# Kernel optimization log

Hardware: AMD Instinct MI355X
Metric: run time of the kernel (lower is better)

Reference implementation:

```python
import jax, jax.numpy as jnp
import numpy as np

B, S, D, R = 8, 2048, 2048, 4  # batch, seq, dim, n_roles


def setup_inputs() -> dict:
    key = jax.random.key(0)
    k1, k2, k3 = jax.random.split(key, 3)
    hidden = jax.random.normal(k1, (B, S, D), dtype=jnp.float32)
    roles = jax.random.randint(k2, (B,), 0, R)
    role_onehot = jax.nn.one_hot(roles, R, dtype=jnp.float32)  # [B, R]
    # per-role Linear params (nn.Linear(dim, dim)), Kaiming-ish init scale
    W = jax.random.normal(k3, (R, D, D), dtype=jnp.float32) / np.sqrt(D)
    b = jnp.zeros((R, D), dtype=jnp.float32)
    scales = jnp.ones((R,), dtype=jnp.float32)  # role_scales
    return {"hidden": hidden, "role_onehot": role_onehot, "W": W, "b": b, "scales": scales}


def reference(hidden, role_onehot, W, b, scales):
    # Training path: compute every role's Linear+Tanh*scale, then mask-sum by one-hot.
    # transformed: [R, B, S, D]
    t = jnp.tanh(jnp.einsum('bsd,rde->rbse', hidden, W) + b[:, None, None, :])
    t = t * scales[:, None, None, None]
    # weights = role_onehot^T broadcast over (S, D); sum over roles
    return jnp.einsum('rbse,br->bse', t, role_onehot)
```

## Files before the change

kernel.cpp:

```cpp
#include <hip/hip_runtime.h>
#include <stdint.h>


#define BDIM 8
#define SDIM 2048
#define DDIM 2048
#define RDIM 4

typedef __attribute__((ext_vector_type(8))) short bf16x8;
typedef __attribute__((ext_vector_type(4))) float f32x4;
typedef unsigned int uint32;

__device__ __forceinline__ unsigned short f2bf(float f) {
    uint32 u = __float_as_uint(f);
    u += 0x7fffu + ((u >> 16) & 1u);
    return (unsigned short)(u >> 16);
}
__device__ __forceinline__ uint32 pack2(float lo, float hi) {
    return (uint32)f2bf(lo) | ((uint32)f2bf(hi) << 16);
}
__device__ __forceinline__ float fast_tanh(float x) {
    float ax = __builtin_fabsf(x);
    float e = __expf(-2.0f * ax);
    float t = (1.0f - e) * __builtin_amdgcn_rcpf(1.0f + e);
    return __builtin_copysignf(t, x);
}


__global__ __launch_bounds__(256) void cvt_h_kernel(const float* __restrict__ h,
                                                    unsigned short* __restrict__ o, int n8) {
    int i = blockIdx.x * blockDim.x + threadIdx.x;
    int stride = gridDim.x * blockDim.x;
    for (; i < n8; i += stride) {
        float4 v0 = reinterpret_cast<const float4*>(h)[2 * i];
        float4 v1 = reinterpret_cast<const float4*>(h)[2 * i + 1];
        uint4 p;
        p.x = pack2(v0.x, v0.y);
        p.y = pack2(v0.z, v0.w);
        p.z = pack2(v1.x, v1.y);
        p.w = pack2(v1.z, v1.w);
        reinterpret_cast<uint4*>(o)[i] = p;
    }
}

__global__ __launch_bounds__(256) void cvt_wt_kernel(const float* __restrict__ w,
                                                     unsigned short* __restrict__ o) {
    __shared__ unsigned short tile[64][65];
    int r = blockIdx.z;
    int e0 = blockIdx.x * 64, d0 = blockIdx.y * 64;
    const float* wr = w + (size_t)r * DDIM * DDIM;
    unsigned short* orr = o + (size_t)r * DDIM * DDIM;
    int tx = threadIdx.x & 63, ty = threadIdx.x >> 6;
    #pragma unroll
    for (int i = ty; i < 64; i += 4)
        tile[i][tx] = f2bf(wr[(size_t)(d0 + i) * DDIM + e0 + tx]);
    __syncthreads();
    #pragma unroll
    for (int i = ty; i < 64; i += 4)
        orr[(size_t)(e0 + i) * DDIM + d0 + tx] = tile[tx][i];
}


__global__ __launch_bounds__(512, 2) void role_gemm8(
    const unsigned short* __restrict__ Hb,
    const unsigned short* __restrict__ Wt,
    const float* __restrict__ onehot,
    const float* __restrict__ bias,
    const float* __restrict__ scales,
    float* __restrict__ out)
{
    constexpr int NT = DDIM / 64;
    extern __shared__ char lds[];

    const int tid = threadIdx.x;
    const int l = tid & 63;
    const int wv = tid >> 6;
    const int wm = wv >> 2;
    const int wn = wv & 3;
    const int fr = l & 15;
    const int fq = l >> 4;
    const int l7 = l & 7;
    const int colx0 = ((fq ^ l7) << 4);
    const int colx1 = (((4 + fq) ^ l7) << 4);

    int bid = blockIdx.x;
    int swz = (bid & 7) * 64 + (bid >> 3);
    int batch = swz >> 6;
    int tt = swz & 63;
    int row0 = (tt >> 3) * 256;
    int n0 = (tt & 7) * 256;

    int role = 0;
    #pragma unroll
    for (int r = 1; r < RDIM; ++r) role = (onehot[batch * RDIM + r] > 0.5f) ? r : role;

    const unsigned short* A = Hb + (size_t)batch * SDIM * DDIM;
    const unsigned short* Bw = Wt + (size_t)role * DDIM * DDIM;

    f32x4 acc[8][4];
    #pragma unroll
    for (int m = 0; m < 8; ++m)
        #pragma unroll
        for (int n = 0; n < 4; ++n)
            #pragma unroll
            for (int j = 0; j < 4; ++j) acc[m][n][j] = 0.0f;

    bf16x8 aR[4][2];
    bf16x8 bQ0[2][2];
    bf16x8 bQ1[2][2];

    auto stage_half = [&](int d, int kind, int h, int T) {
        const unsigned short* sb = kind ? Bw : A;
        int rowbase = (kind ? n0 : row0) + h * 128;
        char* base = lds + d * 65536 + kind * 32768 + h * 16384;
        #pragma unroll
        for (int j = 0; j < 2; ++j) {
            int c = j * 512 + tid;
            int r = c >> 3, kc = c & 7;
            int kcs = kc ^ (r & 7);
            const unsigned short* src = sb + (size_t)(rowbase + r) * DDIM + T * 64 + kcs * 8;
            char* dst = base + ((j * 512 + (tid & 0x1C0)) << 4);
            __builtin_amdgcn_global_load_lds(
                (const __attribute__((address_space(1))) void*)src,
                (__attribute__((address_space(3))) void*)dst, 16, 0, 0);
        }
    };

    auto loadA = [&](int d, int mq) {
        const char* ab = lds + d * 65536;
        #pragma unroll
        for (int mf = 0; mf < 4; ++mf) {
            int rb = (wm * 128 + (mq * 4 + mf) * 16 + fr) * 128;
            aR[mf][0] = *reinterpret_cast<const bf16x8*>(ab + rb + colx0);
            aR[mf][1] = *reinterpret_cast<const bf16x8*>(ab + rb + colx1);
        }
    };
    auto loadB = [&](int d, int nq, bf16x8 (&bR)[2][2]) {
        const char* bb = lds + d * 65536 + 32768;
        #pragma unroll
        for (int nf = 0; nf < 2; ++nf) {
            int rb = (wn * 64 + (nq * 2 + nf) * 16 + fr) * 128;
            bR[nf][0] = *reinterpret_cast<const bf16x8*>(bb + rb + colx0);
            bR[nf][1] = *reinterpret_cast<const bf16x8*>(bb + rb + colx1);
        }
    };
    auto mmaQ = [&](int mq, int nq, bf16x8 (&bR)[2][2]) {
        __builtin_amdgcn_s_setprio(1);
        #pragma unroll
        for (int mf = 0; mf < 4; ++mf)
            #pragma unroll
            for (int nf = 0; nf < 2; ++nf)
                #pragma unroll
                for (int ks = 0; ks < 2; ++ks)
                    acc[mq * 4 + mf][nq * 2 + nf] = __builtin_amdgcn_mfma_f32_16x16x32_bf16(
                        aR[mf][ks], bR[nf][ks], acc[mq * 4 + mf][nq * 2 + nf], 0, 0, 0);
        __builtin_amdgcn_s_setprio(0);
    };

    stage_half(0, 1, 0, 0); stage_half(0, 1, 1, 0);
    stage_half(0, 0, 0, 0); stage_half(0, 0, 1, 0);
    stage_half(1, 1, 0, 1); stage_half(1, 1, 1, 1);
    stage_half(1, 0, 0, 1);
    asm volatile("s_waitcnt vmcnt(6)" ::: "memory");
    __builtin_amdgcn_s_barrier();

    for (int t = 0; t < NT; ++t) {
        const int d = t & 1, e = d ^ 1;
        loadA(d, 0);
        loadB(d, 0, bQ0);
        if (t + 1 < NT) stage_half(e, 0, 1, t + 1);
        __builtin_amdgcn_s_barrier();
        asm volatile("s_waitcnt lgkmcnt(0)" ::: "memory");
        mmaQ(0, 0, bQ0);
        __builtin_amdgcn_s_barrier();
        loadB(d, 1, bQ1);
        __builtin_amdgcn_s_barrier();
        asm volatile("s_waitcnt lgkmcnt(0)" ::: "memory");
        mmaQ(0, 1, bQ1);
        __builtin_amdgcn_s_barrier();
        loadA(d, 1);
        if (t + 2 < NT) stage_half(d, 1, 0, t + 2);
        __builtin_amdgcn_s_barrier();
        asm volatile("s_waitcnt lgkmcnt(0)" ::: "memory");
        mmaQ(1, 1, bQ1);
        __builtin_amdgcn_s_barrier();
        if (t + 2 < NT) { stage_half(d, 1, 1, t + 2); stage_half(d, 0, 0, t + 2); }
        __builtin_amdgcn_s_barrier();
        mmaQ(1, 0, bQ0);
        if (t < NT - 2) { asm volatile("s_waitcnt vmcnt(6)" ::: "memory"); }
        else            { asm volatile("s_waitcnt vmcnt(0)" ::: "memory"); }
        __builtin_amdgcn_s_barrier();
    }

    float sc = scales[role];
    const float* bp = bias + (size_t)role * DDIM + n0 + wn * 64;
    float bb[4];
    #pragma unroll
    for (int nfg = 0; nfg < 4; ++nfg) bb[nfg] = bp[nfg * 16 + fr];
    float* ob = out + ((size_t)batch * SDIM + row0 + wm * 128) * DDIM + n0 + wn * 64;
    #pragma unroll
    for (int mfg = 0; mfg < 8; ++mfg) {
        #pragma unroll
        for (int nfg = 0; nfg < 4; ++nfg) {
            int col = nfg * 16 + fr;
            #pragma unroll
            for (int j = 0; j < 4; ++j) {
                int row = mfg * 16 + fq * 4 + j;
                ob[(size_t)row * DDIM + col] = fast_tanh(acc[mfg][nfg][j] + bb[nfg]) * sc;
            }
        }
    }
}

__global__ __launch_bounds__(256, 2) void role_gemm_fb(
    const float* __restrict__ Ap, const float* __restrict__ Bp,
    const float* __restrict__ onehot, const float* __restrict__ bias,
    const float* __restrict__ scales, float* __restrict__ out)
{
    constexpr int BK = 32;
    constexpr int NT = DDIM / BK;
    constexpr int ROWB = BK * 2 + 16;
    constexpr int TILEB = 128 * ROWB;
    __shared__ char lds[2 * 2 * 128 * 80];

    const unsigned tid = threadIdx.x;
    const int l = tid & 63;
    const int w = tid >> 6;
    const int wm = w >> 1, wn = w & 1;
    const int fr = l & 15, fq = l >> 4;

    int bid = blockIdx.x;
    int swz = (bid & 7) * 256 + (bid >> 3);
    int batch = swz >> 8;
    int tt = swz & 255;
    int row0 = (tt >> 4) * 128;
    int n0 = (tt & 15) * 128;

    int role = 0;
    #pragma unroll
    for (int r = 1; r < RDIM; ++r) role = (onehot[batch * RDIM + r] > 0.5f) ? r : role;

    f32x4 acc[4][4];
    #pragma unroll
    for (int a = 0; a < 4; ++a)
        #pragma unroll
        for (int b2 = 0; b2 < 4; ++b2)
            #pragma unroll
            for (int r = 0; r < 4; ++r) acc[a][b2][r] = 0.0f;

    auto compute = [&](int p) {
        const char* as = lds + p * (2 * TILEB);
        const char* bs = as + TILEB;
        bf16x8 af[4], bf[4];
        #pragma unroll
        for (int a = 0; a < 4; ++a)
            af[a] = *reinterpret_cast<const bf16x8*>(as + (wm * 64 + a * 16 + fr) * ROWB + fq * 16);
        #pragma unroll
        for (int b2 = 0; b2 < 4; ++b2)
            bf[b2] = *reinterpret_cast<const bf16x8*>(bs + (wn * 64 + b2 * 16 + fr) * ROWB + fq * 16);
        #pragma unroll
        for (int a = 0; a < 4; ++a)
            #pragma unroll
            for (int b2 = 0; b2 < 4; ++b2)
                acc[a][b2] = __builtin_amdgcn_mfma_f32_16x16x32_bf16(af[a], bf[b2], acc[a][b2], 0, 0, 0);
    };

    const float* A = Ap + (size_t)batch * SDIM * DDIM;
    const float* Bb = Bp + (size_t)role * DDIM * DDIM;
    const int am = (int)(tid >> 3);
    const int ak = (int)(tid & 7) * 4;
    const int bn = (int)(tid & 127);
    const int bk0 = (int)(tid >> 7) * 4;

    float4 ar[4];
    float br[16];
    auto loadregs = [&](int k0) {
        #pragma unroll
        for (int i = 0; i < 4; ++i)
            ar[i] = *reinterpret_cast<const float4*>(A + (size_t)(row0 + am + 32 * i) * DDIM + k0 + ak);
        #pragma unroll
        for (int i = 0; i < 4; ++i)
            #pragma unroll
            for (int j = 0; j < 4; ++j)
                br[i * 4 + j] = Bb[(size_t)(k0 + bk0 + 8 * i + j) * DDIM + n0 + bn];
    };
    auto writelds = [&](int p) {
        char* as = lds + p * (2 * TILEB);
        char* bs = as + TILEB;
        #pragma unroll
        for (int i = 0; i < 4; ++i) {
            uint2 u;
            u.x = pack2(ar[i].x, ar[i].y);
            u.y = pack2(ar[i].z, ar[i].w);
            *reinterpret_cast<uint2*>(as + (am + 32 * i) * ROWB + ak * 2) = u;
        }
        #pragma unroll
        for (int i = 0; i < 4; ++i) {
            uint2 u;
            u.x = pack2(br[i * 4 + 0], br[i * 4 + 1]);
            u.y = pack2(br[i * 4 + 2], br[i * 4 + 3]);
            *reinterpret_cast<uint2*>(bs + bn * ROWB + (bk0 + 8 * i) * 2) = u;
        }
    };

    loadregs(0);
    writelds(0);
    __syncthreads();
    for (int t = 0; t < NT; ++t) {
        if (t + 1 < NT) loadregs((t + 1) * BK);
        compute(t & 1);
        if (t + 1 < NT) writelds((t + 1) & 1);
        __syncthreads();
    }

    float sc = scales[role];
    const float* bp2 = bias + (size_t)role * DDIM;
    float* outb = out + ((size_t)batch * SDIM + row0) * DDIM + n0;
    #pragma unroll
    for (int a = 0; a < 4; ++a) {
        #pragma unroll
        for (int b2 = 0; b2 < 4; ++b2) {
            int col = wn * 64 + b2 * 16 + fr;
            float bb = bp2[n0 + col];
            #pragma unroll
            for (int r = 0; r < 4; ++r) {
                int row = wm * 64 + a * 16 + fq * 4 + r;
                outb[(size_t)row * DDIM + col] = fast_tanh(acc[a][b2][r] + bb) * sc;
            }
        }
    }
}

extern "C" void kernel_launch(void* const* d_in, const int* in_sizes, int n_in,
                              void* d_out, int out_size, void* d_ws, size_t ws_size,
                              hipStream_t stream) {
    const float* hidden = (const float*)d_in[0];
    const float* onehot = (const float*)d_in[1];
    const float* W      = (const float*)d_in[2];
    const float* bias   = (const float*)d_in[3];
    const float* scales = (const float*)d_in[4];
    float* out = (float*)d_out;

    const size_t needH = (size_t)BDIM * SDIM * DDIM * 2;
    const size_t needW = (size_t)RDIM * DDIM * DDIM * 2;

    if (d_ws != nullptr && ws_size >= needH + needW) {
        unsigned short* Hbf = (unsigned short*)d_ws;
        unsigned short* Wt  = (unsigned short*)((char*)d_ws + needH);
        cvt_h_kernel<<<2048, 256, 0, stream>>>(hidden, Hbf, BDIM * SDIM * DDIM / 8);
        cvt_wt_kernel<<<dim3(DDIM / 64, DDIM / 64, RDIM), dim3(256), 0, stream>>>(W, Wt);
        role_gemm8<<<512, 512, 131072, stream>>>(Hbf, Wt, onehot, bias, scales, out);
    } else {
        role_gemm_fb<<<2048, 256, 0, stream>>>(hidden, W, onehot, bias, scales, out);
    }
}
```

Baseline: 403.8 us.

## Double-buffer A fragments in registers and prefetch next tile's LDS reads

Restructures the main GEMM loop so two register sets of A fragments (aE/aO) alternate, and the next tile's first A/B fragments are read from LDS while the current tile's MFMAs run. Partial lgkmcnt waits and sched_barriers replace the full lgkmcnt(0) waits, and A/B staging is reordered into whole-tile stageA/stageB calls. The goal is to hide LDS read latency behind matrix-core work. It costs more VGPRs under the 512x2 launch bound, which risks spills or lower occupancy.

```diff
diff --git a/kernel.cpp b/kernel.cpp
--- a/kernel.cpp
+++ b/kernel.cpp
@@ -60,8 +60,7 @@
         orr[(size_t)(e0 + i) * DDIM + d0 + tx] = tile[tx][i];
 }
 
-
-__global__ __launch_bounds__(512, 2) void role_gemm8(
+__global__ __launch_bounds__(512, 2) void role_gemm8b(
     const unsigned short* __restrict__ Hb,
     const unsigned short* __restrict__ Wt,
     const float* __restrict__ onehot,
@@ -105,7 +104,8 @@
             #pragma unroll
             for (int j = 0; j < 4; ++j) acc[m][n][j] = 0.0f;
 
-    bf16x8 aR[4][2];
+    bf16x8 aE[4][2];
+    bf16x8 aO[4][2];
     bf16x8 bQ0[2][2];
     bf16x8 bQ1[2][2];
 
@@ -125,26 +125,28 @@
                 (__attribute__((address_space(3))) void*)dst, 16, 0, 0);
         }
     };
-
-    auto loadA = [&](int d, int mq) {
+    auto stageB = [&](int d, int T) { stage_half(d, 1, 0, T); stage_half(d, 1, 1, T); };
+    auto stageA = [&](int d, int T) { stage_half(d, 0, 0, T); stage_half(d, 0, 1, T); };
+
+    auto readA = [&](int d, bf16x8 (&dst)[4][2], int mq) {
         const char* ab = lds + d * 65536;
         #pragma unroll
         for (int mf = 0; mf < 4; ++mf) {
             int rb = (wm * 128 + (mq * 4 + mf) * 16 + fr) * 128;
-            aR[mf][0] = *reinterpret_cast<const bf16x8*>(ab + rb + colx0);
-            aR[mf][1] = *reinterpret_cast<const bf16x8*>(ab + rb + colx1);
-        }
-    };
-    auto loadB = [&](int d, int nq, bf16x8 (&bR)[2][2]) {
+            dst[mf][0] = *reinterpret_cast<const bf16x8*>(ab + rb + colx0);
+            dst[mf][1] = *reinterpret_cast<const bf16x8*>(ab + rb + colx1);
+        }
+    };
+    auto readB = [&](int d, bf16x8 (&dst)[2][2], int nq) {
         const char* bb = lds + d * 65536 + 32768;
         #pragma unroll
         for (int nf = 0; nf < 2; ++nf) {
             int rb = (wn * 64 + (nq * 2 + nf) * 16 + fr) * 128;
-            bR[nf][0] = *reinterpret_cast<const bf16x8*>(bb + rb + colx0);
-            bR[nf][1] = *reinterpret_cast<const bf16x8*>(bb + rb + colx1);
-        }
-    };
-    auto mmaQ = [&](int mq, int nq, bf16x8 (&bR)[2][2]) {
+            dst[nf][0] = *reinterpret_cast<const bf16x8*>(bb + rb + colx0);
+            dst[nf][1] = *reinterpret_cast<const bf16x8*>(bb + rb + colx1);
+        }
+    };
+    auto mmaQ = [&](bf16x8 (&a)[4][2], bf16x8 (&b)[2][2], int mq, int nq) {
         __builtin_amdgcn_s_setprio(1);
         #pragma unroll
         for (int mf = 0; mf < 4; ++mf)
@@ -153,42 +155,48 @@
                 #pragma unroll
                 for (int ks = 0; ks < 2; ++ks)
                     acc[mq * 4 + mf][nq * 2 + nf] = __builtin_amdgcn_mfma_f32_16x16x32_bf16(
-                        aR[mf][ks], bR[nf][ks], acc[mq * 4 + mf][nq * 2 + nf], 0, 0, 0);
+                        a[mf][ks], b[nf][ks], acc[mq * 4 + mf][nq * 2 + nf], 0, 0, 0);
         __builtin_amdgcn_s_setprio(0);
     };
 
-    stage_half(0, 1, 0, 0); stage_half(0, 1, 1, 0);
-    stage_half(0, 0, 0, 0); stage_half(0, 0, 1, 0);
-    stage_half(1, 1, 0, 1); stage_half(1, 1, 1, 1);
-    stage_half(1, 0, 0, 1);
-    asm volatile("s_waitcnt vmcnt(6)" ::: "memory");
+    stageB(0, 0); stageA(0, 0);
+    stageB(1, 1); stageA(1, 1);
+    asm volatile("s_waitcnt vmcnt(8)" ::: "memory");
     __builtin_amdgcn_s_barrier();
+    readB(0, bQ0, 0);
+    readA(0, aE, 0);
 
     for (int t = 0; t < NT; ++t) {
         const int d = t & 1, e = d ^ 1;
-        loadA(d, 0);
-        loadB(d, 0, bQ0);
-        if (t + 1 < NT) stage_half(e, 0, 1, t + 1);
+        readA(d, aO, 1);
+        asm volatile("s_waitcnt lgkmcnt(8)" ::: "memory");
+        __builtin_amdgcn_sched_barrier(0);
+        mmaQ(aE, bQ0, 0, 0);
         __builtin_amdgcn_s_barrier();
-        asm volatile("s_waitcnt lgkmcnt(0)" ::: "memory");
-        mmaQ(0, 0, bQ0);
+        readB(d, bQ1, 1);
+        asm volatile("s_waitcnt lgkmcnt(4)" ::: "memory");
+        __builtin_amdgcn_sched_barrier(0);
+        mmaQ(aO, bQ0, 1, 0);
         __builtin_amdgcn_s_barrier();
-        loadB(d, 1, bQ1);
+        if (t + 1 < NT) {
+            asm volatile("s_waitcnt vmcnt(4)" ::: "memory");
+            __builtin_amdgcn_s_barrier();
+            readB(e, bQ0, 0);
+        }
+        if (t + 2 < NT) stageB(d, t + 2);
+        if (t + 1 < NT) { asm volatile("s_waitcnt lgkmcnt(4)" ::: "memory"); }
+        else            { asm volatile("s_waitcnt lgkmcnt(0)" ::: "memory"); }
+        __builtin_amdgcn_sched_barrier(0);
+        mmaQ(aE, bQ1, 0, 1);
         __builtin_amdgcn_s_barrier();
-        asm volatile("s_waitcnt lgkmcnt(0)" ::: "memory");
-        mmaQ(0, 1, bQ1);
-        __builtin_amdgcn_s_barrier();
-        loadA(d, 1);
-        if (t + 2 < NT) stage_half(d, 1, 0, t + 2);
-        __builtin_amdgcn_s_barrier();
-        asm volatile("s_waitcnt lgkmcnt(0)" ::: "memory");
-        mmaQ(1, 1, bQ1);
-        __builtin_amdgcn_s_barrier();
-        if (t + 2 < NT) { stage_half(d, 1, 1, t + 2); stage_half(d, 0, 0, t + 2); }
-        __builtin_amdgcn_s_barrier();
-        mmaQ(1, 0, bQ0);
-        if (t < NT - 2) { asm volatile("s_waitcnt vmcnt(6)" ::: "memory"); }
-        else            { asm volatile("s_waitcnt vmcnt(0)" ::: "memory"); }
+        if (t + 1 < NT) {
+            if (t + 2 < NT) { asm volatile("s_waitcnt vmcnt(4)" ::: "memory"); }
+            else            { asm volatile("s_waitcnt vmcnt(0)" ::: "memory"); }
+            __builtin_amdgcn_s_barrier();
+            readA(e, aE, 0);
+        }
+        if (t + 2 < NT) stageA(d, t + 2);
+        mmaQ(aO, bQ1, 1, 1);
         __builtin_amdgcn_s_barrier();
     }
 
@@ -349,7 +357,7 @@
         unsigned short* Wt  = (unsigned short*)((char*)d_ws + needH);
         cvt_h_kernel<<<2048, 256, 0, stream>>>(hidden, Hbf, BDIM * SDIM * DDIM / 8);
         cvt_wt_kernel<<<dim3(DDIM / 64, DDIM / 64, RDIM), dim3(256), 0, stream>>>(W, Wt);
-        role_gemm8<<<512, 512, 131072, stream>>>(Hbf, Wt, onehot, bias, scales, out);
+        role_gemm8b<<<512, 512, 131072, stream>>>(Hbf, Wt, onehot, bias, scales, out);
     } else {
         role_gemm_fb<<<2048, 256, 0, stream>>>(hidden, W, onehot, bias, scales, out);
     }
```

Result: no change. 398.8 us (-1.2%).
